# Optimization experiments

Hardware: AMD Instinct MI355X
Metric: run time of the kernel (lower is better)

The kernel has to match this reference:

```python
import jax, jax.numpy as jnp
import numpy as np

N = 10000
E = 320000


def spmm(edge_row, edge_col, edge_val, support):
    # out[r] = sum_{edges (r,c)} val * support[c]  -- torch.spmm(adj, support)
    gathered = support[edge_col] * edge_val[:, None]  # [E, d]
    return jax.ops.segment_sum(gathered, edge_row, num_segments=N)


def setup_inputs() -> dict:
    key = jax.random.key(0)
    ks = jax.random.split(key, 10)
    nfeat, nhid, classes = 512, 512, 256
    return {
        "x": jax.random.normal(ks[0], (N, nfeat), dtype=jnp.float32),
        "edge_row": jax.random.randint(ks[1], (E,), 0, N, dtype=jnp.int32),
        "edge_col": jax.random.randint(ks[2], (E,), 0, N, dtype=jnp.int32),
        "edge_val": jax.random.uniform(ks[3], (E,), dtype=jnp.float32),
        "W0": jax.random.normal(ks[4], (nfeat, nhid), dtype=jnp.float32) / np.sqrt(nfeat),
        "W1": jax.random.normal(ks[5], (2 * nhid, nhid), dtype=jnp.float32) / np.sqrt(2 * nhid),
        "W2": jax.random.normal(ks[6], (2 * nhid, classes), dtype=jnp.float32) / np.sqrt(2 * nhid),
        "b0": jax.random.normal(ks[7], (nhid,), dtype=jnp.float32) * 0.02,
        "b1": jax.random.normal(ks[8], (nhid,), dtype=jnp.float32) * 0.02,
        "b2": jax.random.normal(ks[9], (classes,), dtype=jnp.float32) * 0.02,
    }


def reference(x, edge_row, edge_col, edge_val, W0, W1, W2, b0, b1, b2):
    # layer 0: Linear(nfeat, nhid, bias=False) -> spmm -> +bias
    x_ = spmm(edge_row, edge_col, edge_val, x @ W0) + b0
    h = jax.nn.relu(x_)
    x = jnp.concatenate([h, x_], axis=-1)  # skip=True concat
    # layer 1: Linear(2*nhid, nhid, bias=False) -> spmm -> +bias
    x_ = spmm(edge_row, edge_col, edge_val, x @ W1) + b1
    h = jax.nn.relu(x_)
    x = jnp.concatenate([h, x_], axis=-1)
    # final layer: Linear(2*nhid, classes, bias=False) -> spmm -> +bias
    out = spmm(edge_row, edge_col, edge_val, x @ W2) + b2
    return out
```

## Files before the change

### kernel.cpp

```cpp
#include <hip/hip_runtime.h>
#include <hip/hip_bf16.h>
#include <stdint.h>
#include <type_traits>


typedef _Float16 half8 __attribute__((ext_vector_type(8)));
typedef _Float16 half4 __attribute__((ext_vector_type(4)));
typedef float    f32x4 __attribute__((ext_vector_type(4)));

#define N_NODES 10000
#define M_PAD   10112
#define N_EDGES 320000

__device__ __forceinline__ void async16(const void* g, void* l) {
    __builtin_amdgcn_global_load_lds(
        (const __attribute__((address_space(1))) void*)g,
        (__attribute__((address_space(3))) void*)l, 16, 0, 0);
}

#define PREP_XB   5000
#define PREP_W0B  256
#define PREP_W1B  512
#define PREP_W2B  256
#define PREP_ZB   40
#define PREP_BLKS (PREP_XB + PREP_W0B + PREP_W1B + PREP_W2B + PREP_ZB)

__device__ __forceinline__ void tile_tr(const float* __restrict__ W,
                                        _Float16* __restrict__ Wt,
                                        int K, int Nc, int tR, int tC, int t) {
    __shared__ float tile[32][33];
    const int ty = t >> 5, tx = t & 31;
#pragma unroll
    for (int it = 0; it < 4; ++it)
        tile[ty + 8 * it][tx] = W[(size_t)(tR * 32 + ty + 8 * it) * Nc + tC * 32 + tx];
    __syncthreads();
#pragma unroll
    for (int it = 0; it < 4; ++it)
        Wt[(size_t)(tC * 32 + ty + 8 * it) * K + tR * 32 + tx] =
            (_Float16)tile[tx][ty + 8 * it];
}

__global__ __launch_bounds__(256) void prep(
    const float* __restrict__ x,  _Float16* __restrict__ Xh,
    const float* __restrict__ W0, _Float16* __restrict__ W0t,
    const float* __restrict__ W1, _Float16* __restrict__ W1t,
    const float* __restrict__ W2, _Float16* __restrict__ W2t,
    int* __restrict__ counts) {
    const int t = threadIdx.x;
    int b = blockIdx.x;
    if (b < PREP_XB) {
        int i = b * 256 + t;
        f32x4 v = *(const f32x4*)(x + (size_t)i * 4);
        half4 h;
        h[0] = (_Float16)v[0]; h[1] = (_Float16)v[1];
        h[2] = (_Float16)v[2]; h[3] = (_Float16)v[3];
        *(half4*)(Xh + (size_t)i * 4) = h;
        return;
    }
    b -= PREP_XB;
    if (b < PREP_W0B) { tile_tr(W0, W0t, 512, 512, b >> 4, b & 15, t); return; }
    b -= PREP_W0B;
    if (b < PREP_W1B) { tile_tr(W1, W1t, 1024, 512, b >> 4, b & 15, t); return; }
    b -= PREP_W1B;
    if (b < PREP_W2B) { tile_tr(W2, W2t, 1024, 256, b >> 3, b & 7, t); return; }
    b -= PREP_W2B;
    {
        int i = b * 256 + t;
        if (i < N_NODES) counts[i] = 0;
    }
}

__global__ void hist_rows(const int* __restrict__ rows, int* __restrict__ counts, int E) {
    int i = blockIdx.x * blockDim.x + threadIdx.x;
    if (i < E) atomicAdd(&counts[rows[i]], 1);
}

__global__ __launch_bounds__(1024) void scan_rowptr(
    const int* __restrict__ counts,
    int* __restrict__ row_ptr,
    int* __restrict__ cursor) {
    const int t = threadIdx.x, lane = t & 63, wid = t >> 6;
    const int base = t * 10;
    int c[10];
    int s = 0;
    if (base < N_NODES) {
#pragma unroll
        for (int j = 0; j < 10; ++j) { s += counts[base + j]; c[j] = s; }
    }
    int v = s;
#pragma unroll
    for (int d = 1; d < 64; d <<= 1) {
        int u = __shfl_up(v, d, 64);
        if (lane >= d) v += u;
    }
    __shared__ int wsum[16];
    if (lane == 63) wsum[wid] = v;
    __syncthreads();
    if (t == 0) {
        int run = 0;
#pragma unroll
        for (int i = 0; i < 16; ++i) { int x = wsum[i]; wsum[i] = run; run += x; }
    }
    __syncthreads();
    if (base < N_NODES) {
        const int excl = wsum[wid] + v - s;
        row_ptr[base] = excl; cursor[base] = excl;
#pragma unroll
        for (int j = 1; j < 10; ++j) {
            int val = excl + c[j - 1];
            row_ptr[base + j] = val; cursor[base + j] = val;
        }
    }
    if (t == 0) row_ptr[N_NODES] = N_EDGES;
}

__global__ void scatter_edges(const int* __restrict__ rows,
                              const int* __restrict__ cols,
                              const float* __restrict__ vals,
                              int* __restrict__ cursor,
                              float2* __restrict__ ev, int E) {
    int i = blockIdx.x * blockDim.x + threadIdx.x;
    if (i < E) {
        int r = rows[i];
        int p = atomicAdd(&cursor[r], 1);
        ev[p] = make_float2(__int_as_float(cols[i]), vals[i]);
    }
}

template <int TM, int TN>
__global__ __launch_bounds__(256) void gemm_f16_t(
    const _Float16* __restrict__ A,
    const _Float16* __restrict__ Bt,
    _Float16* __restrict__ C,
    int K, int Nc)
{
    constexpr int WM = TM / 2;
    constexpr int WN = TN / 2;
    constexpr int MT = WM / 16;
    constexpr int NT = WN / 16;
    constexpr int NCHUNK = (TM + TN) / 16;
    constexpr int CA = TM / 16;

    __shared__ _Float16 As[2][TM * 32];
    __shared__ _Float16 Bs[2][TN * 32];

    const int t    = threadIdx.x;
    const int lane = t & 63;
    const int wid  = t >> 6;
    const int wrow = wid >> 1;
    const int wcol = wid & 1;
    const int quad = lane >> 4;
    const int l15  = lane & 15;

    const int rowBase = blockIdx.y * TM;
    const int colBase = blockIdx.x * TN;

    const int rIn = lane >> 2;
    const int cIn = (lane & 3) * 8;

    f32x4 acc[MT][NT];
#pragma unroll
    for (int m = 0; m < MT; ++m)
#pragma unroll
        for (int n = 0; n < NT; ++n)
            acc[m][n] = (f32x4){0.f, 0.f, 0.f, 0.f};

    auto stage = [&](int buf, int k0) {
#pragma unroll
        for (int p = 0; p < NCHUNK / 4; ++p) {
            const int c = wid + p * 4;
            if (c < CA) {
                const int r = c * 16 + rIn;
                async16(&A[(size_t)(rowBase + r) * K + k0 + cIn], &As[buf][c * 512]);
            } else {
                const int r = (c - CA) * 16 + rIn;
                async16(&Bt[(size_t)(colBase + r) * K + k0 + cIn], &Bs[buf][(c - CA) * 512]);
            }
        }
    };

    const int nk = K >> 5;
    stage(0, 0);

    for (int i = 0; i < nk; ++i) {
        __syncthreads();
        if (i + 1 < nk) stage((i + 1) & 1, (i + 1) << 5);

        const int b = i & 1;
        half8 af[MT], bf[NT];
#pragma unroll
        for (int m = 0; m < MT; ++m)
            af[m] = *(const half8*)(&As[b][(wrow * WM + m * 16 + l15) * 32 + quad * 8]);
#pragma unroll
        for (int n = 0; n < NT; ++n)
            bf[n] = *(const half8*)(&Bs[b][(wcol * WN + n * 16 + l15) * 32 + quad * 8]);

#pragma unroll
        for (int m = 0; m < MT; ++m)
#pragma unroll
            for (int n = 0; n < NT; ++n)
                acc[m][n] = __builtin_amdgcn_mfma_f32_16x16x32_f16(
                    af[m], bf[n], acc[m][n], 0, 0, 0);
    }

#pragma unroll
    for (int m = 0; m < MT; ++m) {
#pragma unroll
        for (int n = 0; n < NT; ++n) {
            int col = colBase + wcol * WN + n * 16 + l15;
#pragma unroll
            for (int r = 0; r < 4; ++r) {
                int row = rowBase + wrow * WM + m * 16 + quad * 4 + r;
                C[(size_t)row * Nc + col] = (_Float16)acc[m][n][r];
            }
        }
    }
}

template <int D, bool FINAL>
__global__ __launch_bounds__(256) void spmm_slice(
    const int* __restrict__ row_ptr,
    const float2* __restrict__ ev,
    const _Float16* __restrict__ S,
    const float* __restrict__ bias,
    _Float16* __restrict__ Hout,
    float* __restrict__ Fout)
{
    constexpr int NS = D / 128;
    const int s  = blockIdx.x & (NS - 1);
    const int rq = blockIdx.x / NS;
    const int w  = threadIdx.x >> 6;
    const int row = rq * 4 + w;
    const int lane = threadIdx.x & 63;
    const int g = lane >> 4;
    const int l = lane & 15;

    const int r0 = row_ptr[row];
    const int r1 = row_ptr[row + 1];

    float acc[8];
#pragma unroll
    for (int j = 0; j < 8; ++j) acc[j] = 0.f;

    const _Float16* __restrict__ Sb = S + s * 128 + l * 8;

    int e = r0 + g;
    for (; e + 12 < r1; e += 16) {
        float2 p[4];
        half8  v[4];
#pragma unroll
        for (int u = 0; u < 4; ++u) p[u] = ev[e + 4 * u];
#pragma unroll
        for (int u = 0; u < 4; ++u)
            v[u] = *(const half8*)(Sb + (size_t)__float_as_int(p[u].x) * D);
#pragma unroll
        for (int u = 0; u < 4; ++u)
#pragma unroll
            for (int j = 0; j < 8; ++j) acc[j] += p[u].y * (float)v[u][j];
    }
    for (; e + 4 < r1; e += 8) {
        float2 p0 = ev[e];
        float2 p1 = ev[e + 4];
        half8 v0 = *(const half8*)(Sb + (size_t)__float_as_int(p0.x) * D);
        half8 v1 = *(const half8*)(Sb + (size_t)__float_as_int(p1.x) * D);
#pragma unroll
        for (int j = 0; j < 8; ++j) {
            acc[j] += p0.y * (float)v0[j];
            acc[j] += p1.y * (float)v1[j];
        }
    }
    if (e < r1) {
        float2 p0 = ev[e];
        half8 v0 = *(const half8*)(Sb + (size_t)__float_as_int(p0.x) * D);
#pragma unroll
        for (int j = 0; j < 8; ++j) acc[j] += p0.y * (float)v0[j];
    }

#pragma unroll
    for (int j = 0; j < 8; ++j) {
        acc[j] += __shfl_xor(acc[j], 16, 64);
        acc[j] += __shfl_xor(acc[j], 32, 64);
    }

    const int f0 = s * 128 + l * 8;
    f32x4 b0 = *(const f32x4*)(bias + f0);
    f32x4 b1 = *(const f32x4*)(bias + f0 + 4);

    if constexpr (FINAL) {
        if (g == 0) {
            f32x4 o = {acc[0] + b0[0], acc[1] + b0[1], acc[2] + b0[2], acc[3] + b0[3]};
            *(f32x4*)(Fout + (size_t)row * D + f0) = o;
        } else if (g == 1) {
            f32x4 o = {acc[4] + b1[0], acc[5] + b1[1], acc[6] + b1[2], acc[7] + b1[3]};
            *(f32x4*)(Fout + (size_t)row * D + f0 + 4) = o;
        }
    } else {
        float v[8];
#pragma unroll
        for (int j = 0; j < 4; ++j) v[j] = acc[j] + b0[j];
#pragma unroll
        for (int j = 0; j < 4; ++j) v[4 + j] = acc[4 + j] + b1[j];
        if (g == 0) {
            half8 h;
#pragma unroll
            for (int j = 0; j < 8; ++j) h[j] = (_Float16)(v[j] > 0.f ? v[j] : 0.f);
            *(half8*)(Hout + (size_t)row * (2 * D) + f0) = h;
        } else if (g == 1) {
            half8 h;
#pragma unroll
            for (int j = 0; j < 8; ++j) h[j] = (_Float16)v[j];
            *(half8*)(Hout + (size_t)row * (2 * D) + D + f0) = h;
        }
    }
}

static inline char* alignp(char* p, size_t a) {
    return (char*)(((uintptr_t)p + a - 1) & ~(uintptr_t)(a - 1));
}

extern "C" void kernel_launch(void* const* d_in, const int* in_sizes, int n_in,
                              void* d_out, int out_size, void* d_ws, size_t ws_size,
                              hipStream_t stream) {
    const float* x        = (const float*)d_in[0];
    const int*   edge_row = (const int*)d_in[1];
    const int*   edge_col = (const int*)d_in[2];
    const float* edge_val = (const float*)d_in[3];
    const float* W0 = (const float*)d_in[4];
    const float* W1 = (const float*)d_in[5];
    const float* W2 = (const float*)d_in[6];
    const float* b0 = (const float*)d_in[7];
    const float* b1 = (const float*)d_in[8];
    const float* b2 = (const float*)d_in[9];
    float* out = (float*)d_out;

    const int E = N_EDGES;

    char* p = (char*)d_ws;
    _Float16* Xh  = (_Float16*)alignp(p, 256);  p = (char*)(Xh  + (size_t)M_PAD * 512);
    _Float16* S   = (_Float16*)alignp(p, 256);  p = (char*)(S   + (size_t)M_PAD * 512);
    _Float16* H   = (_Float16*)alignp(p, 256);  p = (char*)(H   + (size_t)M_PAD * 1024);
    _Float16* W0t = (_Float16*)alignp(p, 256);  p = (char*)(W0t + (size_t)512 * 512);
    _Float16* W1t = (_Float16*)alignp(p, 256);  p = (char*)(W1t + (size_t)512 * 1024);
    _Float16* W2t = (_Float16*)alignp(p, 256);  p = (char*)(W2t + (size_t)256 * 1024);
    int*    counts  = (int*)alignp(p, 256);     p = (char*)(counts  + N_NODES);
    int*    row_ptr = (int*)alignp(p, 256);     p = (char*)(row_ptr + N_NODES + 1);
    int*    cursor  = (int*)alignp(p, 256);     p = (char*)(cursor  + N_NODES);
    float2* ev      = (float2*)alignp(p, 256);  p = (char*)(ev      + E);

    prep<<<PREP_BLKS, 256, 0, stream>>>(x, Xh, W0, W0t, W1, W1t, W2, W2t, counts);
    hist_rows<<<(E + 255) / 256, 256, 0, stream>>>(edge_row, counts, E);
    scan_rowptr<<<1, 1024, 0, stream>>>(counts, row_ptr, cursor);
    scatter_edges<<<(E + 255) / 256, 256, 0, stream>>>(edge_row, edge_col, edge_val,
                                                       cursor, ev, E);

    gemm_f16_t<64, 128><<<dim3(4, M_PAD / 64), 256, 0, stream>>>(Xh, W0t, S, 512, 512);
    spmm_slice<512, false><<<(N_NODES / 4) * 4, 256, 0, stream>>>(row_ptr, ev, S, b0, H, nullptr);
    gemm_f16_t<64, 128><<<dim3(4, M_PAD / 64), 256, 0, stream>>>(H, W1t, S, 1024, 512);
    spmm_slice<512, false><<<(N_NODES / 4) * 4, 256, 0, stream>>>(row_ptr, ev, S, b1, H, nullptr);
    gemm_f16_t<64, 64><<<dim3(4, M_PAD / 64), 256, 0, stream>>>(H, W2t, S, 1024, 256);
    spmm_slice<256, true><<<(N_NODES / 4) * 2, 256, 0, stream>>>(row_ptr, ev, S, b2, nullptr, out);
}
```

Before: 272.4 us.

## Merge histogram into prep and fuse edge scatter with first GEMM launch

```diff
diff --git a/kernel.cpp b/kernel.cpp
--- a/kernel.cpp
+++ b/kernel.cpp
@@ -18,117 +18,9 @@
         (__attribute__((address_space(3))) void*)l, 16, 0, 0);
 }
 
-#define PREP_XB   5000
-#define PREP_W0B  256
-#define PREP_W1B  512
-#define PREP_W2B  256
-#define PREP_ZB   40
-#define PREP_BLKS (PREP_XB + PREP_W0B + PREP_W1B + PREP_W2B + PREP_ZB)
-
-__device__ __forceinline__ void tile_tr(const float* __restrict__ W,
-                                        _Float16* __restrict__ Wt,
-                                        int K, int Nc, int tR, int tC, int t) {
-    __shared__ float tile[32][33];
-    const int ty = t >> 5, tx = t & 31;
-#pragma unroll
-    for (int it = 0; it < 4; ++it)
-        tile[ty + 8 * it][tx] = W[(size_t)(tR * 32 + ty + 8 * it) * Nc + tC * 32 + tx];
-    __syncthreads();
-#pragma unroll
-    for (int it = 0; it < 4; ++it)
-        Wt[(size_t)(tC * 32 + ty + 8 * it) * K + tR * 32 + tx] =
-            (_Float16)tile[tx][ty + 8 * it];
-}
-
-__global__ __launch_bounds__(256) void prep(
-    const float* __restrict__ x,  _Float16* __restrict__ Xh,
-    const float* __restrict__ W0, _Float16* __restrict__ W0t,
-    const float* __restrict__ W1, _Float16* __restrict__ W1t,
-    const float* __restrict__ W2, _Float16* __restrict__ W2t,
-    int* __restrict__ counts) {
-    const int t = threadIdx.x;
-    int b = blockIdx.x;
-    if (b < PREP_XB) {
-        int i = b * 256 + t;
-        f32x4 v = *(const f32x4*)(x + (size_t)i * 4);
-        half4 h;
-        h[0] = (_Float16)v[0]; h[1] = (_Float16)v[1];
-        h[2] = (_Float16)v[2]; h[3] = (_Float16)v[3];
-        *(half4*)(Xh + (size_t)i * 4) = h;
-        return;
-    }
-    b -= PREP_XB;
-    if (b < PREP_W0B) { tile_tr(W0, W0t, 512, 512, b >> 4, b & 15, t); return; }
-    b -= PREP_W0B;
-    if (b < PREP_W1B) { tile_tr(W1, W1t, 1024, 512, b >> 4, b & 15, t); return; }
-    b -= PREP_W1B;
-    if (b < PREP_W2B) { tile_tr(W2, W2t, 1024, 256, b >> 3, b & 7, t); return; }
-    b -= PREP_W2B;
-    {
-        int i = b * 256 + t;
-        if (i < N_NODES) counts[i] = 0;
-    }
-}
-
-__global__ void hist_rows(const int* __restrict__ rows, int* __restrict__ counts, int E) {
-    int i = blockIdx.x * blockDim.x + threadIdx.x;
-    if (i < E) atomicAdd(&counts[rows[i]], 1);
-}
-
-__global__ __launch_bounds__(1024) void scan_rowptr(
-    const int* __restrict__ counts,
-    int* __restrict__ row_ptr,
-    int* __restrict__ cursor) {
-    const int t = threadIdx.x, lane = t & 63, wid = t >> 6;
-    const int base = t * 10;
-    int c[10];
-    int s = 0;
-    if (base < N_NODES) {
-#pragma unroll
-        for (int j = 0; j < 10; ++j) { s += counts[base + j]; c[j] = s; }
-    }
-    int v = s;
-#pragma unroll
-    for (int d = 1; d < 64; d <<= 1) {
-        int u = __shfl_up(v, d, 64);
-        if (lane >= d) v += u;
-    }
-    __shared__ int wsum[16];
-    if (lane == 63) wsum[wid] = v;
-    __syncthreads();
-    if (t == 0) {
-        int run = 0;
-#pragma unroll
-        for (int i = 0; i < 16; ++i) { int x = wsum[i]; wsum[i] = run; run += x; }
-    }
-    __syncthreads();
-    if (base < N_NODES) {
-        const int excl = wsum[wid] + v - s;
-        row_ptr[base] = excl; cursor[base] = excl;
-#pragma unroll
-        for (int j = 1; j < 10; ++j) {
-            int val = excl + c[j - 1];
-            row_ptr[base + j] = val; cursor[base + j] = val;
-        }
-    }
-    if (t == 0) row_ptr[N_NODES] = N_EDGES;
-}
-
-__global__ void scatter_edges(const int* __restrict__ rows,
-                              const int* __restrict__ cols,
-                              const float* __restrict__ vals,
-                              int* __restrict__ cursor,
-                              float2* __restrict__ ev, int E) {
-    int i = blockIdx.x * blockDim.x + threadIdx.x;
-    if (i < E) {
-        int r = rows[i];
-        int p = atomicAdd(&cursor[r], 1);
-        ev[p] = make_float2(__int_as_float(cols[i]), vals[i]);
-    }
-}
-
 template <int TM, int TN>
-__global__ __launch_bounds__(256) void gemm_f16_t(
+__device__ __forceinline__ void gemm_body(
+    int bx, int by,
     const _Float16* __restrict__ A,
     const _Float16* __restrict__ Bt,
     _Float16* __restrict__ C,
@@ -152,8 +44,8 @@
     const int quad = lane >> 4;
     const int l15  = lane & 15;
 
-    const int rowBase = blockIdx.y * TM;
-    const int colBase = blockIdx.x * TN;
+    const int rowBase = by * TM;
+    const int colBase = bx * TN;
 
     const int rIn = lane >> 2;
     const int cIn = (lane & 3) * 8;
@@ -214,6 +106,133 @@
                 C[(size_t)row * Nc + col] = (_Float16)acc[m][n][r];
             }
         }
+    }
+}
+
+template <int TM, int TN>
+__global__ __launch_bounds__(256) void gemm_f16_t(
+    const _Float16* __restrict__ A,
+    const _Float16* __restrict__ Bt,
+    _Float16* __restrict__ C,
+    int K, int Nc)
+{
+    gemm_body<TM, TN>(blockIdx.x, blockIdx.y, A, Bt, C, K, Nc);
+}
+
+#define PREP_XB   5000
+#define PREP_W0B  256
+#define PREP_W1B  512
+#define PREP_W2B  256
+#define HIST_B    1250
+#define PREPH_BLKS (PREP_XB + PREP_W0B + PREP_W1B + PREP_W2B + HIST_B)
+
+__device__ __forceinline__ void tile_tr(const float* __restrict__ W,
+                                        _Float16* __restrict__ Wt,
+                                        int K, int Nc, int tR, int tC, int t) {
+    __shared__ float tile[32][33];
+    const int ty = t >> 5, tx = t & 31;
+#pragma unroll
+    for (int it = 0; it < 4; ++it)
+        tile[ty + 8 * it][tx] = W[(size_t)(tR * 32 + ty + 8 * it) * Nc + tC * 32 + tx];
+    __syncthreads();
+#pragma unroll
+    for (int it = 0; it < 4; ++it)
+        Wt[(size_t)(tC * 32 + ty + 8 * it) * K + tR * 32 + tx] =
+            (_Float16)tile[tx][ty + 8 * it];
+}
+
+__global__ __launch_bounds__(256) void prep_hist(
+    const float* __restrict__ x,  _Float16* __restrict__ Xh,
+    const float* __restrict__ W0, _Float16* __restrict__ W0t,
+    const float* __restrict__ W1, _Float16* __restrict__ W1t,
+    const float* __restrict__ W2, _Float16* __restrict__ W2t,
+    const int* __restrict__ edge_row, int* __restrict__ counts) {
+    const int t = threadIdx.x;
+    int b = blockIdx.x;
+    if (b < PREP_XB) {
+        int i = b * 256 + t;
+        f32x4 v = *(const f32x4*)(x + (size_t)i * 4);
+        half4 h;
+        h[0] = (_Float16)v[0]; h[1] = (_Float16)v[1];
+        h[2] = (_Float16)v[2]; h[3] = (_Float16)v[3];
+        *(half4*)(Xh + (size_t)i * 4) = h;
+        return;
+    }
+    b -= PREP_XB;
+    if (b < PREP_W0B) { tile_tr(W0, W0t, 512, 512, b >> 4, b & 15, t); return; }
+    b -= PREP_W0B;
+    if (b < PREP_W1B) { tile_tr(W1, W1t, 1024, 512, b >> 4, b & 15, t); return; }
+    b -= PREP_W1B;
+    if (b < PREP_W2B) { tile_tr(W2, W2t, 1024, 256, b >> 3, b & 7, t); return; }
+    b -= PREP_W2B;
+    {
+        int i = b * 256 + t;
+        if (i < N_EDGES) atomicAdd(&counts[edge_row[i]], 1);
+    }
+}
+
+__global__ __launch_bounds__(1024) void scan_rowptr(
+    const int* __restrict__ counts,
+    int* __restrict__ row_ptr,
+    int* __restrict__ cursor) {
+    const int t = threadIdx.x, lane = t & 63, wid = t >> 6;
+    const int base = t * 10;
+    int c[10];
+    int s = 0;
+    if (base < N_NODES) {
+#pragma unroll
+        for (int j = 0; j < 10; ++j) { s += counts[base + j]; c[j] = s; }
+    }
+    int v = s;
+#pragma unroll
+    for (int d = 1; d < 64; d <<= 1) {
+        int u = __shfl_up(v, d, 64);
+        if (lane >= d) v += u;
+    }
+    __shared__ int wsum[16];
+    if (lane == 63) wsum[wid] = v;
+    __syncthreads();
+    if (t == 0) {
+        int run = 0;
+#pragma unroll
+        for (int i = 0; i < 16; ++i) { int x = wsum[i]; wsum[i] = run; run += x; }
+    }
+    __syncthreads();
+    if (base < N_NODES) {
+        const int excl = wsum[wid] + v - s;
+        row_ptr[base] = excl; cursor[base] = excl;
+#pragma unroll
+        for (int j = 1; j < 10; ++j) {
+            int val = excl + c[j - 1];
+            row_ptr[base + j] = val; cursor[base + j] = val;
+        }
+    }
+    if (t == 0) row_ptr[N_NODES] = N_EDGES;
+}
+
+#define G0_BLKS 632
+#define SCAT_BLKS 1250
+
+__global__ __launch_bounds__(256) void gemm0_scatter(
+    const _Float16* __restrict__ Xh,
+    const _Float16* __restrict__ W0t,
+    _Float16* __restrict__ S,
+    const int* __restrict__ rows,
+    const int* __restrict__ cols,
+    const float* __restrict__ vals,
+    int* __restrict__ cursor,
+    float2* __restrict__ ev) {
+    int b = blockIdx.x;
+    if (b < G0_BLKS) {
+        gemm_body<64, 128>(b & 3, b >> 2, Xh, W0t, S, 512, 512);
+        return;
+    }
+    b -= G0_BLKS;
+    int i = b * 256 + threadIdx.x;
+    if (i < N_EDGES) {
+        int r = rows[i];
+        int p = atomicAdd(&cursor[r], 1);
+        ev[p] = make_float2(__int_as_float(cols[i]), vals[i]);
     }
 }
 
@@ -347,13 +366,13 @@
     int*    cursor  = (int*)alignp(p, 256);     p = (char*)(cursor  + N_NODES);
     float2* ev      = (float2*)alignp(p, 256);  p = (char*)(ev      + E);
 
-    prep<<<PREP_BLKS, 256, 0, stream>>>(x, Xh, W0, W0t, W1, W1t, W2, W2t, counts);
-    hist_rows<<<(E + 255) / 256, 256, 0, stream>>>(edge_row, counts, E);
+    hipMemsetAsync(counts, 0, N_NODES * sizeof(int), stream);
+    prep_hist<<<PREPH_BLKS, 256, 0, stream>>>(x, Xh, W0, W0t, W1, W1t, W2, W2t,
+                                              edge_row, counts);
     scan_rowptr<<<1, 1024, 0, stream>>>(counts, row_ptr, cursor);
-    scatter_edges<<<(E + 255) / 256, 256, 0, stream>>>(edge_row, edge_col, edge_val,
-                                                       cursor, ev, E);
-
-    gemm_f16_t<64, 128><<<dim3(4, M_PAD / 64), 256, 0, stream>>>(Xh, W0t, S, 512, 512);
+
+    gemm0_scatter<<<G0_BLKS + SCAT_BLKS, 256, 0, stream>>>(
+        Xh, W0t, S, edge_row, edge_col, edge_val, cursor, ev);
     spmm_slice<512, false><<<(N_NODES / 4) * 4, 256, 0, stream>>>(row_ptr, ev, S, b0, H, nullptr);
     gemm_f16_t<64, 128><<<dim3(4, M_PAD / 64), 256, 0, stream>>>(H, W1t, S, 1024, 512);
     spmm_slice<512, false><<<(N_NODES / 4) * 4, 256, 0, stream>>>(row_ptr, ev, S, b1, H, nullptr);
```

After: 264.0 us. 3.1% less time.
